# Performance work log

Hardware: AMD Instinct MI355X
Metric: run time of the kernel (lower is better)

The kernel has to match this reference:

```python
import jax, jax.numpy as jnp
import numpy as np

B, S, D = 2, 1024, 2048
H, KV, HD = 16, 4, 128
GROUPS = H // KV
THETA = 10000.0


def act_quant(xr, xi):
    # per-token 8-bit absmax quantization over last dim, joint scale for re/im, STE
    amax = jnp.maximum(jnp.max(jnp.abs(xr), -1, keepdims=True),
                       jnp.max(jnp.abs(xi), -1, keepdims=True))
    s = 127.0 / jnp.maximum(amax, 1e-5)
    qr = jnp.clip(jnp.round(xr * s), -128, 127) / s
    qi = jnp.clip(jnp.round(xi * s), -128, 127) / s
    return xr + jax.lax.stop_gradient(qr - xr), xi + jax.lax.stop_gradient(qi - xi)


def weight_quant(wr, wi):
    # Fairy+-i direction quantization: each weight -> scale * d, d in {+1,-1,+i,-i}; STE
    mag = jnp.mean(jnp.sqrt(wr * wr + wi * wi))
    use_re = jnp.abs(wr) >= jnp.abs(wi)
    qr = jnp.where(use_re, jnp.sign(wr) * mag, 0.0)
    qi = jnp.where(use_re, 0.0, jnp.sign(wi) * mag)
    return wr + jax.lax.stop_gradient(qr - wr), wi + jax.lax.stop_gradient(qi - wi)


def complex_linear(xr, xi, wr, wi):
    xr, xi = act_quant(xr, xi)
    wr, wi = weight_quant(wr, wi)
    o_re = xr @ wr - xi @ wi
    o_im = xr @ wi + xi @ wr
    return o_re, o_im


def rotate_half(x):
    h = x.shape[-1] // 2
    return jnp.concatenate([-x[..., h:], x[..., :h]], axis=-1)


def rope_tables():
    inv_freq = 1.0 / (THETA ** (jnp.arange(0, HD, 2, dtype=jnp.float32) / HD))
    pos = jnp.arange(S, dtype=jnp.float32)
    freqs = pos[:, None] * inv_freq[None, :]          # [S, HD/2]
    emb = jnp.concatenate([freqs, freqs], axis=-1)    # [S, HD]
    return jnp.cos(emb)[None, None], jnp.sin(emb)[None, None]  # [1,1,S,HD]


def _heads(x, n):
    # [B,S,n*HD] -> [B,n,S,HD]
    return x.reshape(B, S, n, HD).transpose(0, 2, 1, 3)


def _attn(hidden_real, hidden_imag, wq_re, wq_im, wk_re, wk_im,
          wv_re, wv_im, wo_re, wo_im):
    q_re, q_im = complex_linear(hidden_real, hidden_imag, wq_re, wq_im)
    k_re, k_im = complex_linear(hidden_real, hidden_imag, wk_re, wk_im)
    v_re, v_im = complex_linear(hidden_real, hidden_imag, wv_re, wv_im)

    q_re, q_im = _heads(q_re, H), _heads(q_im, H)      # [B,H,S,HD]
    k_re, k_im = _heads(k_re, KV), _heads(k_im, KV)    # [B,KV,S,HD]
    v_re, v_im = _heads(v_re, KV), _heads(v_im, KV)

    cos, sin = rope_tables()
    # RoPE applied only to real components of q and k
    q_re = q_re * cos + rotate_half(q_re) * sin
    k_re = k_re * cos + rotate_half(k_re) * sin

    # GQA repeat
    k_re = jnp.repeat(k_re, GROUPS, axis=1)
    k_im = jnp.repeat(k_im, GROUPS, axis=1)
    v_re = jnp.repeat(v_re, GROUPS, axis=1)
    v_im = jnp.repeat(v_im, GROUPS, axis=1)

    # real scores = Re(q . conj(k)) = q_re.k_re + q_im.k_im
    scores = (jnp.einsum('bhqd,bhkd->bhqk', q_re, k_re) +
              jnp.einsum('bhqd,bhkd->bhqk', q_im, k_im)) / jnp.sqrt(jnp.float32(HD))
    causal = jnp.tril(jnp.ones((S, S), dtype=bool))
    scores = jnp.where(causal[None, None], scores, jnp.finfo(scores.dtype).min)
    attn = jax.nn.softmax(scores, axis=-1)

    o_re = jnp.einsum('bhqk,bhkd->bhqd', attn, v_re)
    o_im = jnp.einsum('bhqk,bhkd->bhqd', attn, v_im)
    o_re = o_re.transpose(0, 2, 1, 3).reshape(B, S, H * HD)
    o_im = o_im.transpose(0, 2, 1, 3).reshape(B, S, H * HD)

    out_re, out_im = complex_linear(o_re, o_im, wo_re, wo_im)
    return jnp.stack([out_re, out_im])  # [2,B,S,D]


def setup_inputs() -> dict:
    key = jax.random.key(0)
    ks = jax.random.split(key, 12)
    w = lambda k, shp: jax.random.normal(k, shp, dtype=jnp.float32) * 0.02
    return {
        'hidden_real': jax.random.normal(ks[0], (B, S, D), dtype=jnp.float32),
        'hidden_imag': jax.random.normal(ks[1], (B, S, D), dtype=jnp.float32),
        'wq_re': w(ks[2], (D, H * HD)), 'wq_im': w(ks[3], (D, H * HD)),
        'wk_re': w(ks[4], (D, KV * HD)), 'wk_im': w(ks[5], (D, KV * HD)),
        'wv_re': w(ks[6], (D, KV * HD)), 'wv_im': w(ks[7], (D, KV * HD)),
        'wo_re': w(ks[8], (H * HD, D)), 'wo_im': w(ks[9], (H * HD, D)),
    }


def reference(hidden_real, hidden_imag, wq_re, wq_im, wk_re, wk_im,
              wv_re, wv_im, wo_re, wo_im):
    return _attn(hidden_real, hidden_imag, wq_re, wq_im, wk_re, wk_im,
                 wv_re, wv_im, wo_re, wo_im)
```

## Files before the change

kernel.cpp:

```cpp
#include <hip/hip_runtime.h>
#include <stdint.h>

#define B_   2
#define S_   1024
#define D_   2048
#define H_   16
#define KV_  4
#define HD_  128
#define NTOK (B_ * S_)
#define QD   (H_ * HD_)
#define KD   (KV_ * HD_)

using i32x4  = __attribute__((ext_vector_type(4)))  int;
using i32x16 = __attribute__((ext_vector_type(16))) int;
using f32x4  = __attribute__((ext_vector_type(4)))  float;
using bf16x8 = __attribute__((ext_vector_type(8)))  short;

#define LN1E4_OVER_64 0.14391156831212725f

__device__ __forceinline__ float bf2f(uint16_t u) { return __uint_as_float((uint32_t)u << 16); }
__device__ __forceinline__ uint16_t f2bf(float f) {
    uint32_t u = __float_as_uint(f);
    return (uint16_t)((u + 0x7FFFu + ((u >> 16) & 1u)) >> 16);
}

__global__ __launch_bounds__(256)
void act_quant_i8_kernel(const float* __restrict__ xr, const float* __restrict__ xi,
                         int8_t* __restrict__ qr, int8_t* __restrict__ qi,
                         float* __restrict__ invs)
{
    const int tok = blockIdx.x, t = threadIdx.x;
    const float* pr = xr + (size_t)tok * 2048 + t * 8;
    const float* pi = xi + (size_t)tok * 2048 + t * 8;
    float4 r0 = *(const float4*)pr, r1 = *(const float4*)(pr + 4);
    float4 i0 = *(const float4*)pi, i1 = *(const float4*)(pi + 4);
    float am = fmaxf(fmaxf(fmaxf(fabsf(r0.x), fabsf(r0.y)), fmaxf(fabsf(r0.z), fabsf(r0.w))),
                     fmaxf(fmaxf(fabsf(r1.x), fabsf(r1.y)), fmaxf(fabsf(r1.z), fabsf(r1.w))));
    am = fmaxf(am, fmaxf(fmaxf(fmaxf(fabsf(i0.x), fabsf(i0.y)), fmaxf(fabsf(i0.z), fabsf(i0.w))),
                         fmaxf(fmaxf(fabsf(i1.x), fabsf(i1.y)), fmaxf(fabsf(i1.z), fabsf(i1.w)))));
    __shared__ float red[256];
    red[t] = am;
    __syncthreads();
    for (int st = 128; st > 0; st >>= 1) {
        if (t < st) red[t] = fmaxf(red[t], red[t + st]);
        __syncthreads();
    }
    const float s = 127.0f / fmaxf(red[0], 1e-5f);
    if (t == 0) invs[tok] = 1.0f / s;
#define Q8(x) ((uint32_t)(uint8_t)(int8_t)(int)fminf(fmaxf(rintf((x) * s), -128.f), 127.f))
    uint32_t a0 = Q8(r0.x) | (Q8(r0.y) << 8) | (Q8(r0.z) << 16) | (Q8(r0.w) << 24);
    uint32_t a1 = Q8(r1.x) | (Q8(r1.y) << 8) | (Q8(r1.z) << 16) | (Q8(r1.w) << 24);
    uint32_t b0 = Q8(i0.x) | (Q8(i0.y) << 8) | (Q8(i0.z) << 16) | (Q8(i0.w) << 24);
    uint32_t b1 = Q8(i1.x) | (Q8(i1.y) << 8) | (Q8(i1.z) << 16) | (Q8(i1.w) << 24);
#undef Q8
    *(uint32_t*)(qr + (size_t)tok * 2048 + t * 8)     = a0;
    *(uint32_t*)(qr + (size_t)tok * 2048 + t * 8 + 4) = a1;
    *(uint32_t*)(qi + (size_t)tok * 2048 + t * 8)     = b0;
    *(uint32_t*)(qi + (size_t)tok * 2048 + t * 8 + 4) = b1;
}

__global__ __launch_bounds__(256)
void decode_kernel(const float* __restrict__ wr, const float* __restrict__ wi,
                   int N, int8_t* __restrict__ psr, int8_t* __restrict__ psi,
                   int8_t* __restrict__ pnsi, int n_off, float* __restrict__ mag_out)
{
    __shared__ alignas(16) int8_t tr[3][64][80];
    __shared__ float red[256];
    const int n0 = blockIdx.x * 64, k0 = blockIdx.y * 64;
    float msum = 0.f;
    for (int idx = threadIdx.x; idx < 4096; idx += 256) {
        int j = idx & 63, i = idx >> 6;
        size_t g = (size_t)(k0 + i) * N + n0 + j;
        float a = wr[g], b = wi[g];
        msum += sqrtf(a * a + b * b);
        int8_t sr, si;
        if (fabsf(a) >= fabsf(b)) {
            sr = (a > 0.f) ? 1 : ((a < 0.f) ? -1 : 0);
            si = 0;
        } else {
            sr = 0;
            si = (b > 0.f) ? 1 : ((b < 0.f) ? -1 : 0);
        }
        tr[0][j][i] = sr;
        tr[1][j][i] = si;
        tr[2][j][i] = (int8_t)(-si);
    }
    red[threadIdx.x] = msum;
    __syncthreads();
    for (int st = 128; st > 0; st >>= 1) {
        if (threadIdx.x < st) red[threadIdx.x] += red[threadIdx.x + st];
        __syncthreads();
    }
    if (threadIdx.x == 0) atomicAdd(mag_out, red[0]);
    int8_t* planes[3] = { psr, psi, pnsi };
    for (int idx = threadIdx.x; idx < 768; idx += 256) {
        int p = idx >> 8, rem = idx & 255, n = rem >> 2, c = rem & 3;
        int4 v = *(const int4*)&tr[p][n][c * 16];
        *(int4*)(planes[p] + (size_t)(n_off + n0 + n) * 2048 + k0 + c * 16) = v;
    }
}

__device__ __forceinline__ void async_copy16(const void* g, void* l) {
    __builtin_amdgcn_global_load_lds((const __attribute__((address_space(1))) void*)g,
                                     (__attribute__((address_space(3))) void*)l, 16, 0, 0);
}

template <int MODE>
__global__ __launch_bounds__(256)
void gemm_i8_kernel(const int8_t* __restrict__ axr, const int8_t* __restrict__ axi,
                    const int8_t* __restrict__ bsr, const int8_t* __restrict__ bsi,
                    const int8_t* __restrict__ bnsi,
                    int Nout, const float* __restrict__ invs,
                    const float* __restrict__ mag_sums,
                    float magc0, float magc1, float magc2,
                    float* o_re, float* o_im,
                    uint16_t* kbr, uint16_t* kbi, uint16_t* vbr, uint16_t* vbi)
{
    __shared__ alignas(16) int8_t smem[2][5 * 8192];
    const int tid = threadIdx.x;
    const int wav = tid >> 6, lane = tid & 63;
    const int tileM = blockIdx.y * 128, tileN = blockIdx.x * 128;
    const int wm = wav & 1, wn = wav >> 1;
    const int K = 2048;

    const int8_t* gplane[5] = { axr, axi, bsr, bsi, bnsi };
    const int     rbase[5]  = { tileM, tileM, tileN, tileN, tileN };

    i32x16 acc_re[2][2] = {};
    i32x16 acc_im[2][2] = {};

    auto issue_tile = [&](int k0, int buf) {
#pragma unroll
        for (int i = 0; i < 10; ++i) {
            int q = wav + 4 * i;
            int pl = q >> 3, seg = q & 7;
            int c = seg >> 1, m0 = (seg & 1) << 6;
            const int8_t* g = gplane[pl] + (size_t)(rbase[pl] + m0 + lane) * K + k0 + c * 16;
            int8_t* l = &smem[buf][pl * 8192 + (c * 128 + m0) * 16];
            async_copy16(g, l);
        }
    };

    issue_tile(0, 0);
    issue_tile(64, 1);

    for (int k = 0; k < 32; ++k) {
        if (k == 31) { asm volatile("s_waitcnt vmcnt(0)" ::: "memory"); }
        else         { asm volatile("s_waitcnt vmcnt(10)" ::: "memory"); }
        asm volatile("s_barrier" ::: "memory");
        const int8_t* sb = smem[k & 1];
#pragma unroll
        for (int s = 0; s < 2; ++s) {
            const int cc = 2 * s + (lane >> 5);
            const int rA = wm * 64 + (lane & 31);
            const int rB = wn * 64 + (lane & 31);
            i32x4 fxr[2], fxi[2], fsr[2], fsi[2], fns[2];
#pragma unroll
            for (int mb = 0; mb < 2; ++mb) {
                int off = (cc * 128 + rA + mb * 32) * 16;
                fxr[mb] = *(const i32x4*)&sb[0 * 8192 + off];
                fxi[mb] = *(const i32x4*)&sb[1 * 8192 + off];
            }
#pragma unroll
            for (int nb = 0; nb < 2; ++nb) {
                int off = (cc * 128 + rB + nb * 32) * 16;
                fsr[nb] = *(const i32x4*)&sb[2 * 8192 + off];
                fsi[nb] = *(const i32x4*)&sb[3 * 8192 + off];
                fns[nb] = *(const i32x4*)&sb[4 * 8192 + off];
            }
#pragma unroll
            for (int mb = 0; mb < 2; ++mb)
#pragma unroll
                for (int nb = 0; nb < 2; ++nb) {
                    acc_re[mb][nb] = __builtin_amdgcn_mfma_i32_32x32x32_i8(fxr[mb], fsr[nb], acc_re[mb][nb], 0, 0, 0);
                    acc_re[mb][nb] = __builtin_amdgcn_mfma_i32_32x32x32_i8(fxi[mb], fns[nb], acc_re[mb][nb], 0, 0, 0);
                    acc_im[mb][nb] = __builtin_amdgcn_mfma_i32_32x32x32_i8(fxr[mb], fsi[nb], acc_im[mb][nb], 0, 0, 0);
                    acc_im[mb][nb] = __builtin_amdgcn_mfma_i32_32x32x32_i8(fxi[mb], fsr[nb], acc_im[mb][nb], 0, 0, 0);
                }
        }
        asm volatile("s_barrier" ::: "memory");
        if (k + 2 < 32) issue_tile((k + 2) * 64, k & 1);
    }

    const int ln31 = lane & 31, lq = lane >> 5;
#pragma unroll
    for (int mb = 0; mb < 2; ++mb) {
#pragma unroll
        for (int nb = 0; nb < 2; ++nb) {
            const int gn = tileN + wn * 64 + nb * 32 + ln31;
            float mag;
            if (MODE == 0)
                mag = (gn < 2048) ? mag_sums[0] * magc0
                    : (gn < 2560) ? mag_sums[1] * magc1
                                  : mag_sums[2] * magc2;
            else
                mag = mag_sums[0] * magc0;
#pragma unroll
            for (int r = 0; r < 16; ++r) {
                const int row = (r & 3) + 8 * (r >> 2) + 4 * lq;
                const int gm = tileM + wm * 64 + mb * 32 + row;
                const float sc = mag * invs[gm];
                const float re = (float)acc_re[mb][nb][r] * sc;
                const float im = (float)acc_im[mb][nb][r] * sc;
                if (MODE == 1) {
                    o_re[(size_t)gm * Nout + gn] = re;
                    o_im[(size_t)gm * Nout + gn] = im;
                } else {
                    const int s = gm & (S_ - 1), bb = gm >> 10;
                    if (gn < 2048) {
                        o_re[(size_t)gm * 2048 + gn] = re;
                        o_im[(size_t)gm * 2048 + gn] = im;
                    } else if (gn < 2560) {
                        int c = gn - 2048, kvh = c >> 7, d = c & 127;
                        size_t off = ((size_t)(bb * KV_ + kvh) * S_ + s) * 128 + d;
                        kbr[off] = f2bf(re);
                        kbi[off] = f2bf(im);
                    } else {
                        int c = gn - 2560, kvh = c >> 7, d = c & 127;
                        size_t off = ((size_t)(bb * KV_ + kvh) * S_ + s) * 128 + d;
                        vbr[off] = f2bf(re);
                        vbi[off] = f2bf(im);
                    }
                }
            }
        }
    }
}

__global__ __launch_bounds__(256)
void rope_q_kernel(const float* __restrict__ q_re, const float* __restrict__ q_im,
                   uint16_t* __restrict__ qb_re, uint16_t* __restrict__ qb_im)
{
    int gidx = blockIdx.x * 256 + threadIdx.x;
    int j = gidx & 15, h = (gidx >> 4) & 15, tok = gidx >> 8;
    int s = tok & (S_ - 1), b = tok >> 10;
    int d0 = j * 4;
    size_t ib = (size_t)tok * 2048 + h * 128;
    float4 r0 = *(const float4*)&q_re[ib + d0];
    float4 r1 = *(const float4*)&q_re[ib + d0 + 64];
    float4 i0 = *(const float4*)&q_im[ib + d0];
    float4 i1 = *(const float4*)&q_im[ib + d0 + 64];
    float ro0[4], ro1[4];
    float rv0[4] = { r0.x, r0.y, r0.z, r0.w };
    float rv1[4] = { r1.x, r1.y, r1.z, r1.w };
#pragma unroll
    for (int t = 0; t < 4; ++t) {
        float f = __expf(-(float)(d0 + t) * LN1E4_OVER_64);
        float sn, c;
        __sincosf((float)s * f, &sn, &c);
        ro0[t] = rv0[t] * c - rv1[t] * sn;
        ro1[t] = rv1[t] * c + rv0[t] * sn;
    }
    size_t ob = ((size_t)(b * H_ + h) * S_ + s) * 128;
    ushort4 w;
    w = (ushort4){ f2bf(ro0[0]), f2bf(ro0[1]), f2bf(ro0[2]), f2bf(ro0[3]) };
    *(ushort4*)&qb_re[ob + d0] = w;
    w = (ushort4){ f2bf(ro1[0]), f2bf(ro1[1]), f2bf(ro1[2]), f2bf(ro1[3]) };
    *(ushort4*)&qb_re[ob + d0 + 64] = w;
    w = (ushort4){ f2bf(i0.x), f2bf(i0.y), f2bf(i0.z), f2bf(i0.w) };
    *(ushort4*)&qb_im[ob + d0] = w;
    w = (ushort4){ f2bf(i1.x), f2bf(i1.y), f2bf(i1.z), f2bf(i1.w) };
    *(ushort4*)&qb_im[ob + d0 + 64] = w;
}

__global__ __launch_bounds__(256)
void rope_k_kernel(uint16_t* __restrict__ kb_re)
{
    int gidx = blockIdx.x * 256 + threadIdx.x;
    int j = gidx & 15, kvh = (gidx >> 4) & 3;
    int rest = gidx >> 6;
    int s = rest & (S_ - 1), b = rest >> 10;
    int d0 = j * 4;
    size_t base = ((size_t)(b * KV_ + kvh) * S_ + s) * 128;
    ushort4 u0 = *(const ushort4*)&kb_re[base + d0];
    ushort4 u1 = *(const ushort4*)&kb_re[base + d0 + 64];
    float rv0[4] = { bf2f(u0.x), bf2f(u0.y), bf2f(u0.z), bf2f(u0.w) };
    float rv1[4] = { bf2f(u1.x), bf2f(u1.y), bf2f(u1.z), bf2f(u1.w) };
    float ro0[4], ro1[4];
#pragma unroll
    for (int t = 0; t < 4; ++t) {
        float f = __expf(-(float)(d0 + t) * LN1E4_OVER_64);
        float sn, c;
        __sincosf((float)s * f, &sn, &c);
        ro0[t] = rv0[t] * c - rv1[t] * sn;
        ro1[t] = rv1[t] * c + rv0[t] * sn;
    }
    *(ushort4*)&kb_re[base + d0]      = (ushort4){ f2bf(ro0[0]), f2bf(ro0[1]), f2bf(ro0[2]), f2bf(ro0[3]) };
    *(ushort4*)&kb_re[base + d0 + 64] = (ushort4){ f2bf(ro1[0]), f2bf(ro1[1]), f2bf(ro1[2]), f2bf(ro1[3]) };
}

__global__ __launch_bounds__(256)
void vtrans_kernel(const uint16_t* __restrict__ vbr, const uint16_t* __restrict__ vbi,
                   uint16_t* __restrict__ vtr, uint16_t* __restrict__ vti)
{
    __shared__ uint16_t t[32][36];
    const int pl = blockIdx.z & 1, bk = blockIdx.z >> 1;
    const int s0 = blockIdx.x * 32, d0 = blockIdx.y * 32;
    const uint16_t* src = (pl ? vbi : vbr) + ((size_t)bk * S_) * 128;
    uint16_t*       dst = (pl ? vti : vtr) + ((size_t)bk * 128) * S_;
    const int r = threadIdx.x >> 3, c = (threadIdx.x & 7) * 4;
    *(ushort4*)&t[r][c] = *(const ushort4*)&src[(size_t)(s0 + r) * 128 + d0 + c];
    __syncthreads();
    ushort4 o = (ushort4){ t[c][r], t[c + 1][r], t[c + 2][r], t[c + 3][r] };
    *(ushort4*)&dst[(size_t)(d0 + r) * S_ + s0 + c] = o;
}

__global__ __launch_bounds__(256)
void attn_mfma_kernel(const uint16_t* __restrict__ qb_re, const uint16_t* __restrict__ qb_im,
                      const uint16_t* __restrict__ kb_re, const uint16_t* __restrict__ kb_im,
                      const uint16_t* __restrict__ vt_re, const uint16_t* __restrict__ vt_im,
                      float* __restrict__ o_re, float* __restrict__ o_im)
{
    __shared__ alignas(16) uint16_t sk[2][32][136];
    __shared__ alignas(16) uint16_t sv[2][128][40];
    __shared__ alignas(16) uint16_t sp[4][16][40];

    const int tid = threadIdx.x;
    const int w = tid >> 6, lane = tid & 63;
    const int r16 = lane & 15, q4 = lane >> 4;
    const int qt = gridDim.x - 1 - blockIdx.x;
    const int h = blockIdx.y, b = blockIdx.z;
    const int kvh = h >> 2;
    const int q0 = qt * 64, qw0 = q0 + w * 16;

    bf16x8 qfr[4], qfi[4];
    {
        const size_t qbase = ((size_t)(b * H_ + h) * S_ + qw0 + r16) * 128;
#pragma unroll
        for (int ks = 0; ks < 4; ++ks) {
            const int col = ks * 32 + q4 * 8;
            qfr[ks] = *(const bf16x8*)&qb_re[qbase + col];
            qfi[ks] = *(const bf16x8*)&qb_im[qbase + col];
        }
    }

    f32x4 oa[2][8] = {};
    float m_r[4] = { -3e38f, -3e38f, -3e38f, -3e38f };
    float l_r[4] = { 0.f, 0.f, 0.f, 0.f };

    const size_t kgbase0 = (size_t)(b * KV_ + kvh) * S_ * 128;
    const size_t vgbase0 = (size_t)(b * KV_ + kvh) * 128 * (size_t)S_;

    for (int c0 = 0; c0 < q0 + 64; c0 += 32) {
        for (int idx = tid; idx < 1024; idx += 256) {
            int pl = idx >> 9, c = idx & 511, r = c >> 4, ch = c & 15;
            const uint16_t* src = (pl ? kb_im : kb_re) + kgbase0 + (size_t)(c0 + r) * 128 + ch * 8;
            *(uint4*)&sk[pl][r][ch * 8] = *(const uint4*)src;
        }
        for (int idx = tid; idx < 1024; idx += 256) {
            int pl = idx >> 9, c = idx & 511, d = c >> 2, ch = c & 3;
            const uint16_t* src = (pl ? vt_im : vt_re) + vgbase0 + (size_t)d * S_ + c0 + ch * 8;
            *(uint4*)&sv[pl][d][ch * 8] = *(const uint4*)src;
        }
        __syncthreads();

        if (c0 <= qw0 + 15) {
            f32x4 sc[2] = {};
#pragma unroll
            for (int cblk = 0; cblk < 2; ++cblk) {
                const int krow = cblk * 16 + r16;
#pragma unroll
                for (int ks = 0; ks < 4; ++ks) {
                    const int kcol = ks * 32 + q4 * 8;
                    bf16x8 kr = *(const bf16x8*)&sk[0][krow][kcol];
                    bf16x8 ki = *(const bf16x8*)&sk[1][krow][kcol];
                    sc[cblk] = __builtin_amdgcn_mfma_f32_16x16x32_bf16(qfr[ks], kr, sc[cblk], 0, 0, 0);
                    sc[cblk] = __builtin_amdgcn_mfma_f32_16x16x32_bf16(qfi[ks], ki, sc[cblk], 0, 0, 0);
                }
            }
#pragma unroll
            for (int cblk = 0; cblk < 2; ++cblk)
#pragma unroll
                for (int reg = 0; reg < 4; ++reg) {
                    float sval = sc[cblk][reg] * 0.08838834764831845f;
                    const int rowg = qw0 + q4 * 4 + reg;
                    const int colg = c0 + cblk * 16 + r16;
                    if (colg > rowg) sval = -3e38f;
                    sc[cblk][reg] = sval;
                }
            float al[4];
#pragma unroll
            for (int reg = 0; reg < 4; ++reg) {
                float mx = fmaxf(sc[0][reg], sc[1][reg]);
#pragma unroll
                for (int msk = 1; msk < 16; msk <<= 1) mx = fmaxf(mx, __shfl_xor(mx, msk));
                const float mn = fmaxf(m_r[reg], mx);
                al[reg] = __expf(m_r[reg] - mn);
                const float p0 = __expf(sc[0][reg] - mn);
                const float p1 = __expf(sc[1][reg] - mn);
                sc[0][reg] = p0; sc[1][reg] = p1;
                float rs = p0 + p1;
#pragma unroll
                for (int msk = 1; msk < 16; msk <<= 1) rs += __shfl_xor(rs, msk);
                l_r[reg] = l_r[reg] * al[reg] + rs;
                m_r[reg] = mn;
            }
#pragma unroll
            for (int cblk = 0; cblk < 2; ++cblk)
#pragma unroll
                for (int reg = 0; reg < 4; ++reg)
                    sp[w][q4 * 4 + reg][cblk * 16 + r16] = f2bf(sc[cblk][reg]);
#pragma unroll
            for (int dblk = 0; dblk < 8; ++dblk)
#pragma unroll
                for (int reg = 0; reg < 4; ++reg) {
                    oa[0][dblk][reg] *= al[reg];
                    oa[1][dblk][reg] *= al[reg];
                }
            bf16x8 pf = *(const bf16x8*)&sp[w][r16][q4 * 8];
#pragma unroll
            for (int dblk = 0; dblk < 8; ++dblk) {
                const int vrow = dblk * 16 + r16;
                bf16x8 vr = *(const bf16x8*)&sv[0][vrow][q4 * 8];
                bf16x8 vi = *(const bf16x8*)&sv[1][vrow][q4 * 8];
                oa[0][dblk] = __builtin_amdgcn_mfma_f32_16x16x32_bf16(pf, vr, oa[0][dblk], 0, 0, 0);
                oa[1][dblk] = __builtin_amdgcn_mfma_f32_16x16x32_bf16(pf, vi, oa[1][dblk], 0, 0, 0);
            }
        }
        __syncthreads();
    }

    float inv[4];
#pragma unroll
    for (int reg = 0; reg < 4; ++reg) inv[reg] = 1.f / l_r[reg];
#pragma unroll
    for (int dblk = 0; dblk < 8; ++dblk) {
        const int col = h * 128 + dblk * 16 + r16;
#pragma unroll
        for (int reg = 0; reg < 4; ++reg) {
            const size_t tok = (size_t)b * S_ + qw0 + q4 * 4 + reg;
            o_re[tok * 2048 + col] = oa[0][dblk][reg] * inv[reg];
            o_im[tok * 2048 + col] = oa[1][dblk][reg] * inv[reg];
        }
    }
}

extern "C" void kernel_launch(void* const* d_in, const int* in_sizes, int n_in,
                              void* d_out, int out_size, void* d_ws, size_t ws_size,
                              hipStream_t stream)
{
    const float* hr    = (const float*)d_in[0];
    const float* hi    = (const float*)d_in[1];
    const float* wq_re = (const float*)d_in[2];
    const float* wq_im = (const float*)d_in[3];
    const float* wk_re = (const float*)d_in[4];
    const float* wk_im = (const float*)d_in[5];
    const float* wv_re = (const float*)d_in[6];
    const float* wv_im = (const float*)d_in[7];
    const float* wo_re = (const float*)d_in[8];
    const float* wo_im = (const float*)d_in[9];
    float* out = (float*)d_out;
    char*  base = (char*)d_ws;

    const size_t MB4  = (size_t)2048 * 2048;
    const size_t QKVP = (size_t)3072 * 2048;
    const size_t KVE  = (size_t)B_ * KV_ * S_ * 128;

    float*   mags   = (float*)(base);
    float*   invs1  = (float*)(base + 1024);
    float*   invs2  = (float*)(base + 9216);
    int8_t*  xr_q   = (int8_t*)(base + 32768);
    int8_t*  xi_q   = xr_q + MB4;
    int8_t*  qkv_sr = xi_q + MB4;
    int8_t*  qkv_si = qkv_sr + QKVP;
    int8_t*  qkv_ns = qkv_si + QKVP;
    int8_t*  wo_sr  = qkv_ns + QKVP;
    int8_t*  wo_si  = wo_sr + MB4;
    int8_t*  wo_ns  = wo_si + MB4;
    float*   q_re   = (float*)(wo_ns + MB4);
    float*   q_im   = q_re + MB4;
    uint16_t* kb_re = (uint16_t*)(q_im + MB4);
    uint16_t* kb_im = kb_re + KVE;
    uint16_t* vb_re = kb_im + KVE;
    uint16_t* vb_im = vb_re + KVE;
    uint16_t* vt_re = (uint16_t*)xr_q;
    uint16_t* vt_im = (uint16_t*)xi_q;
    uint16_t* qb_re = (uint16_t*)qkv_sr;
    uint16_t* qb_im = (uint16_t*)(qkv_sr + 8388608);

    hipMemsetAsync(mags, 0, 16, stream);

    decode_kernel<<<dim3(32, 32), 256, 0, stream>>>(wq_re, wq_im, 2048, qkv_sr, qkv_si, qkv_ns, 0,    mags + 0);
    decode_kernel<<<dim3(8, 32),  256, 0, stream>>>(wk_re, wk_im, 512,  qkv_sr, qkv_si, qkv_ns, 2048, mags + 1);
    decode_kernel<<<dim3(8, 32),  256, 0, stream>>>(wv_re, wv_im, 512,  qkv_sr, qkv_si, qkv_ns, 2560, mags + 2);
    decode_kernel<<<dim3(32, 32), 256, 0, stream>>>(wo_re, wo_im, 2048, wo_sr, wo_si, wo_ns, 0,       mags + 3);

    act_quant_i8_kernel<<<NTOK, 256, 0, stream>>>(hr, hi, xr_q, xi_q, invs1);

    gemm_i8_kernel<0><<<dim3(24, 16), 256, 0, stream>>>(
        xr_q, xi_q, qkv_sr, qkv_si, qkv_ns, 0, invs1, mags,
        1.0f / (float)((size_t)D_ * QD), 1.0f / (float)((size_t)D_ * KD), 1.0f / (float)((size_t)D_ * KD),
        q_re, q_im, kb_re, kb_im, vb_re, vb_im);

    rope_q_kernel<<<NTOK * H_ * 16 / 256, 256, 0, stream>>>(q_re, q_im, qb_re, qb_im);
    rope_k_kernel<<<NTOK * KV_ * 16 / 256, 256, 0, stream>>>(kb_re);
    vtrans_kernel<<<dim3(S_ / 32, 128 / 32, B_ * KV_ * 2), 256, 0, stream>>>(vb_re, vb_im, vt_re, vt_im);

    attn_mfma_kernel<<<dim3(S_ / 64, H_, B_), 256, 0, stream>>>(
        qb_re, qb_im, kb_re, kb_im, vt_re, vt_im, q_re, q_im);

    act_quant_i8_kernel<<<NTOK, 256, 0, stream>>>(q_re, q_im, xr_q, xi_q, invs2);

    gemm_i8_kernel<1><<<dim3(16, 16), 256, 0, stream>>>(
        xr_q, xi_q, wo_sr, wo_si, wo_ns, 2048, invs2, mags + 3,
        1.0f / (float)((size_t)QD * D_), 0.f, 0.f,
        out, out + MB4, nullptr, nullptr, nullptr, nullptr);
}
```

Baseline: 537.5 us.

## Double-buffer K/V tiles via register prefetch in attention kernel

The attention loop now issues global loads for the next K/V tile into registers before computing on the current tile. It writes them into a second LDS buffer afterwards, so there is one barrier per iteration instead of two. The aim is to hide global load latency behind the MFMA work. It also raises wave priority around the MFMA blocks with s_setprio. The cost is double the LDS use (about 70KB) and extra registers, which may reduce occupancy.

```diff
diff --git a/kernel.cpp b/kernel.cpp
--- a/kernel.cpp
+++ b/kernel.cpp
@@ -311,8 +311,8 @@
                       const uint16_t* __restrict__ vt_re, const uint16_t* __restrict__ vt_im,
                       float* __restrict__ o_re, float* __restrict__ o_im)
 {
-    __shared__ alignas(16) uint16_t sk[2][32][136];
-    __shared__ alignas(16) uint16_t sv[2][128][40];
+    __shared__ alignas(16) uint16_t sk[2][2][32][136];
+    __shared__ alignas(16) uint16_t sv[2][2][128][40];
     __shared__ alignas(16) uint16_t sp[4][16][40];
 
     const int tid = threadIdx.x;
@@ -341,33 +341,66 @@
     const size_t kgbase0 = (size_t)(b * KV_ + kvh) * S_ * 128;
     const size_t vgbase0 = (size_t)(b * KV_ + kvh) * 128 * (size_t)S_;
 
-    for (int c0 = 0; c0 < q0 + 64; c0 += 32) {
-        for (int idx = tid; idx < 1024; idx += 256) {
-            int pl = idx >> 9, c = idx & 511, r = c >> 4, ch = c & 15;
+    const int nk = (q0 + 64) >> 5;
+
+    uint4 kreg[4], vreg[4];
+    auto load_tile = [&](int c0) {
+#pragma unroll
+        for (int i = 0; i < 4; ++i) {
+            const int idx = tid + 256 * i;
+            const int pl = idx >> 9, rem = idx & 511, r = rem >> 4, ch = rem & 15;
             const uint16_t* src = (pl ? kb_im : kb_re) + kgbase0 + (size_t)(c0 + r) * 128 + ch * 8;
-            *(uint4*)&sk[pl][r][ch * 8] = *(const uint4*)src;
-        }
-        for (int idx = tid; idx < 1024; idx += 256) {
-            int pl = idx >> 9, c = idx & 511, d = c >> 2, ch = c & 3;
+            kreg[i] = *(const uint4*)src;
+        }
+#pragma unroll
+        for (int i = 0; i < 4; ++i) {
+            const int idx = tid + 256 * i;
+            const int pl = idx >> 9, rem = idx & 511, d = rem >> 2, ch = rem & 3;
             const uint16_t* src = (pl ? vt_im : vt_re) + vgbase0 + (size_t)d * S_ + c0 + ch * 8;
-            *(uint4*)&sv[pl][d][ch * 8] = *(const uint4*)src;
-        }
-        __syncthreads();
+            vreg[i] = *(const uint4*)src;
+        }
+    };
+    auto write_tile = [&](int buf) {
+#pragma unroll
+        for (int i = 0; i < 4; ++i) {
+            const int idx = tid + 256 * i;
+            const int pl = idx >> 9, rem = idx & 511, r = rem >> 4, ch = rem & 15;
+            *(uint4*)&sk[buf][pl][r][ch * 8] = kreg[i];
+        }
+#pragma unroll
+        for (int i = 0; i < 4; ++i) {
+            const int idx = tid + 256 * i;
+            const int pl = idx >> 9, rem = idx & 511, d = rem >> 2, ch = rem & 3;
+            *(uint4*)&sv[buf][pl][d][ch * 8] = vreg[i];
+        }
+    };
+
+    load_tile(0);
+    write_tile(0);
+    __syncthreads();
+
+    for (int k = 0; k < nk; ++k) {
+        const int c0 = k << 5;
+        const int cur = k & 1;
+        const bool pf = (k + 1 < nk);
+        if (pf) load_tile(c0 + 32);
 
         if (c0 <= qw0 + 15) {
             f32x4 sc[2] = {};
+            __builtin_amdgcn_s_setprio(1);
 #pragma unroll
             for (int cblk = 0; cblk < 2; ++cblk) {
                 const int krow = cblk * 16 + r16;
 #pragma unroll
                 for (int ks = 0; ks < 4; ++ks) {
                     const int kcol = ks * 32 + q4 * 8;
-                    bf16x8 kr = *(const bf16x8*)&sk[0][krow][kcol];
-                    bf16x8 ki = *(const bf16x8*)&sk[1][krow][kcol];
+                    bf16x8 kr = *(const bf16x8*)&sk[cur][0][krow][kcol];
+                    bf16x8 ki = *(const bf16x8*)&sk[cur][1][krow][kcol];
                     sc[cblk] = __builtin_amdgcn_mfma_f32_16x16x32_bf16(qfr[ks], kr, sc[cblk], 0, 0, 0);
                     sc[cblk] = __builtin_amdgcn_mfma_f32_16x16x32_bf16(qfi[ks], ki, sc[cblk], 0, 0, 0);
                 }
             }
+            __builtin_amdgcn_s_setprio(0);
 #pragma unroll
             for (int cblk = 0; cblk < 2; ++cblk)
 #pragma unroll
@@ -407,16 +440,20 @@
                     oa[0][dblk][reg] *= al[reg];
                     oa[1][dblk][reg] *= al[reg];
                 }
-            bf16x8 pf = *(const bf16x8*)&sp[w][r16][q4 * 8];
+            bf16x8 pfr = *(const bf16x8*)&sp[w][r16][q4 * 8];
+            __builtin_amdgcn_s_setprio(1);
 #pragma unroll
             for (int dblk = 0; dblk < 8; ++dblk) {
                 const int vrow = dblk * 16 + r16;
-                bf16x8 vr = *(const bf16x8*)&sv[0][vrow][q4 * 8];
-                bf16x8 vi = *(const bf16x8*)&sv[1][vrow][q4 * 8];
-                oa[0][dblk] = __builtin_amdgcn_mfma_f32_16x16x32_bf16(pf, vr, oa[0][dblk], 0, 0, 0);
-                oa[1][dblk] = __builtin_amdgcn_mfma_f32_16x16x32_bf16(pf, vi, oa[1][dblk], 0, 0, 0);
+                bf16x8 vr = *(const bf16x8*)&sv[cur][0][vrow][q4 * 8];
+                bf16x8 vi = *(const bf16x8*)&sv[cur][1][vrow][q4 * 8];
+                oa[0][dblk] = __builtin_amdgcn_mfma_f32_16x16x32_bf16(pfr, vr, oa[0][dblk], 0, 0, 0);
+                oa[1][dblk] = __builtin_amdgcn_mfma_f32_16x16x32_bf16(pfr, vi, oa[1][dblk], 0, 0, 0);
             }
-        }
+            __builtin_amdgcn_s_setprio(0);
+        }
+
+        if (pf) write_tile(cur ^ 1);
         __syncthreads();
     }
 
```

Result: slower. 568.0 us (+5.7%).

## Split attention KV range into two halves with a separate merge kernel

Applied to the files above, without the earlier changes.

Each attention query tile is now processed by two blocks, each covering half of the causal key range. Each block writes its unnormalized partial outputs plus its running max and sum to workspace. A new merge kernel rescales and combines the two partials. This doubles the grid (from 512 to 1024 blocks) to improve occupancy and load balance. The cost is an extra kernel launch and extra global traffic for the partial outputs.

```diff
diff --git a/kernel.cpp b/kernel.cpp
--- a/kernel.cpp
+++ b/kernel.cpp
@@ -10,6 +10,7 @@
 #define NTOK (B_ * S_)
 #define QD   (H_ * HD_)
 #define KD   (KV_ * HD_)
+#define NROW (B_ * H_ * S_)
 
 using i32x4  = __attribute__((ext_vector_type(4)))  int;
 using i32x16 = __attribute__((ext_vector_type(16))) int;
@@ -309,7 +310,9 @@
 void attn_mfma_kernel(const uint16_t* __restrict__ qb_re, const uint16_t* __restrict__ qb_im,
                       const uint16_t* __restrict__ kb_re, const uint16_t* __restrict__ kb_im,
                       const uint16_t* __restrict__ vt_re, const uint16_t* __restrict__ vt_im,
-                      float* __restrict__ o_re, float* __restrict__ o_im)
+                      float* __restrict__ op_re0, float* __restrict__ op_im0,
+                      float* __restrict__ op_re1, float* __restrict__ op_im1,
+                      float* __restrict__ mlbuf)
 {
     __shared__ alignas(16) uint16_t sk[2][32][136];
     __shared__ alignas(16) uint16_t sv[2][128][40];
@@ -318,7 +321,9 @@
     const int tid = threadIdx.x;
     const int w = tid >> 6, lane = tid & 63;
     const int r16 = lane & 15, q4 = lane >> 4;
-    const int qt = gridDim.x - 1 - blockIdx.x;
+    const int bx = blockIdx.x;
+    const int sp_idx = bx & 1;
+    const int qt = (gridDim.x >> 1) - 1 - (bx >> 1);
     const int h = blockIdx.y, b = blockIdx.z;
     const int kvh = h >> 2;
     const int q0 = qt * 64, qw0 = q0 + w * 16;
@@ -341,7 +346,13 @@
     const size_t kgbase0 = (size_t)(b * KV_ + kvh) * S_ * 128;
     const size_t vgbase0 = (size_t)(b * KV_ + kvh) * 128 * (size_t)S_;
 
-    for (int c0 = 0; c0 < q0 + 64; c0 += 32) {
+    const int nk   = (q0 + 64) >> 5;
+    const int half = nk >> 1;
+    const int kbeg = sp_idx ? half : 0;
+    const int kend = sp_idx ? nk   : half;
+
+    for (int k = kbeg; k < kend; ++k) {
+        const int c0 = k << 5;
         for (int idx = tid; idx < 1024; idx += 256) {
             int pl = idx >> 9, c = idx & 511, r = c >> 4, ch = c & 15;
             const uint16_t* src = (pl ? kb_im : kb_re) + kgbase0 + (size_t)(c0 + r) * 128 + ch * 8;
@@ -420,19 +431,56 @@
         __syncthreads();
     }
 
-    float inv[4];
-#pragma unroll
-    for (int reg = 0; reg < 4; ++reg) inv[reg] = 1.f / l_r[reg];
+    float* opr = sp_idx ? op_re1 : op_re0;
+    float* opi = sp_idx ? op_im1 : op_im0;
 #pragma unroll
     for (int dblk = 0; dblk < 8; ++dblk) {
         const int col = h * 128 + dblk * 16 + r16;
 #pragma unroll
         for (int reg = 0; reg < 4; ++reg) {
             const size_t tok = (size_t)b * S_ + qw0 + q4 * 4 + reg;
-            o_re[tok * 2048 + col] = oa[0][dblk][reg] * inv[reg];
-            o_im[tok * 2048 + col] = oa[1][dblk][reg] * inv[reg];
-        }
-    }
+            opr[tok * 2048 + col] = oa[0][dblk][reg];
+            opi[tok * 2048 + col] = oa[1][dblk][reg];
+        }
+    }
+    if (r16 == 0) {
+        const int rowb = (b * H_ + h) * S_ + qw0 + q4 * 4;
+#pragma unroll
+        for (int reg = 0; reg < 4; ++reg) {
+            mlbuf[sp_idx * NROW + rowb + reg]            = m_r[reg];
+            mlbuf[2 * NROW + sp_idx * NROW + rowb + reg] = l_r[reg];
+        }
+    }
+}
+
+__global__ __launch_bounds__(256)
+void attn_merge_kernel(const float* __restrict__ op_re0, const float* __restrict__ op_im0,
+                       const float* __restrict__ op_re1, const float* __restrict__ op_im1,
+                       const float* __restrict__ mlbuf,
+                       float* __restrict__ o_re, float* __restrict__ o_im)
+{
+    const int gid = blockIdx.x * 256 + threadIdx.x;
+    const int tok = gid >> 9;
+    const int rest = gid & 511, h = rest >> 5, j = rest & 31;
+    const int d0 = j * 4;
+    const int b = tok >> 10, s = tok & (S_ - 1);
+    const int row = (b * H_ + h) * S_ + s;
+    const float m0 = mlbuf[row],            m1 = mlbuf[NROW + row];
+    const float l0 = mlbuf[2 * NROW + row], l1 = mlbuf[3 * NROW + row];
+    const float m  = fmaxf(m0, m1);
+    const float a0 = __expf(m0 - m), a1 = __expf(m1 - m);
+    const float rl = 1.f / (l0 * a0 + l1 * a1);
+    const float c0 = a0 * rl, c1 = a1 * rl;
+    const size_t off = (size_t)tok * 2048 + h * 128 + d0;
+    float4 r0 = *(const float4*)&op_re0[off], r1 = *(const float4*)&op_re1[off];
+    float4 i0 = *(const float4*)&op_im0[off], i1 = *(const float4*)&op_im1[off];
+    float4 ro, io;
+    ro.x = r0.x * c0 + r1.x * c1;  ro.y = r0.y * c0 + r1.y * c1;
+    ro.z = r0.z * c0 + r1.z * c1;  ro.w = r0.w * c0 + r1.w * c1;
+    io.x = i0.x * c0 + i1.x * c1;  io.y = i0.y * c0 + i1.y * c1;
+    io.z = i0.z * c0 + i1.z * c1;  io.w = i0.w * c0 + i1.w * c1;
+    *(float4*)&o_re[off] = ro;
+    *(float4*)&o_im[off] = io;
 }
 
 extern "C" void kernel_launch(void* const* d_in, const int* in_sizes, int n_in,
@@ -473,6 +521,9 @@
     uint16_t* kb_im = kb_re + KVE;
     uint16_t* vb_re = kb_im + KVE;
     uint16_t* vb_im = vb_re + KVE;
+    float*   opr1   = (float*)(vb_im + KVE);
+    float*   opi1   = opr1 + MB4;
+    float*   mlbuf  = opi1 + MB4;
     uint16_t* vt_re = (uint16_t*)xr_q;
     uint16_t* vt_im = (uint16_t*)xi_q;
     uint16_t* qb_re = (uint16_t*)qkv_sr;
@@ -496,8 +547,10 @@
     rope_k_kernel<<<NTOK * KV_ * 16 / 256, 256, 0, stream>>>(kb_re);
     vtrans_kernel<<<dim3(S_ / 32, 128 / 32, B_ * KV_ * 2), 256, 0, stream>>>(vb_re, vb_im, vt_re, vt_im);
 
-    attn_mfma_kernel<<<dim3(S_ / 64, H_, B_), 256, 0, stream>>>(
-        qb_re, qb_im, kb_re, kb_im, vt_re, vt_im, q_re, q_im);
+    attn_mfma_kernel<<<dim3(S_ / 64 * 2, H_, B_), 256, 0, stream>>>(
+        qb_re, qb_im, kb_re, kb_im, vt_re, vt_im,
+        q_re, q_im, opr1, opi1, mlbuf);
+    attn_merge_kernel<<<4096, 256, 0, stream>>>(q_re, q_im, opr1, opi1, mlbuf, q_re, q_im);
 
     act_quant_i8_kernel<<<NTOK, 256, 0, stream>>>(q_re, q_im, xr_q, xi_q, invs2);
 
```

Result: slower. 552.8 us (+2.8%).
